# Performance work log

Hardware: AMD Instinct MI355X
Metric: run time of the kernel (lower is better)

## Reference

```python
import jax, jax.numpy as jnp
import numpy as np

N_NODES = 50000
N_EDGES = 800000
D = 128


def setup_inputs() -> dict:
    key = jax.random.key(0)
    ks = jax.random.split(key, 8)
    h = jax.random.normal(ks[0], (N_NODES, D), dtype=jnp.float32)
    src = jax.random.randint(ks[1], (N_EDGES,), 0, N_NODES, dtype=jnp.int64)
    dst = jax.random.randint(ks[2], (N_EDGES,), 0, N_NODES, dtype=jnp.int64)
    # Glorot-ish init for the three GraphConv weights
    scale = 1.0 / np.sqrt(D)
    W0 = jax.random.normal(ks[3], (D, D), dtype=jnp.float32) * scale
    W1 = jax.random.normal(ks[4], (D, D), dtype=jnp.float32) * scale
    W2 = jax.random.normal(ks[5], (D, D), dtype=jnp.float32) * scale
    b0 = jnp.zeros((D,), dtype=jnp.float32)
    b1 = jnp.zeros((D,), dtype=jnp.float32)
    b2 = jnp.zeros((D,), dtype=jnp.float32)
    return {"h": h, "src": src, "dst": dst, "W0": W0, "b0": b0,
            "W1": W1, "b1": b1, "W2": W2, "b2": b2}


def _graph_conv(x, src, dst, W, b, n_nodes):
    """DGL GraphConv, norm='both', activation=ReLU.
    in_feats == out_feats -> aggregate first, then matmul W."""
    ones = jnp.ones_like(src, dtype=x.dtype)
    out_deg = jnp.clip(jax.ops.segment_sum(ones, src, num_segments=n_nodes), 1.0)
    in_deg = jnp.clip(jax.ops.segment_sum(ones, dst, num_segments=n_nodes), 1.0)
    x = x * (out_deg ** -0.5)[:, None]          # src-side normalization
    m = jax.ops.segment_sum(x[src], dst, num_segments=n_nodes)  # sparse aggregation
    m = m * (in_deg ** -0.5)[:, None]           # dst-side normalization
    return jax.nn.relu(m @ W + b)


def reference(h, src, dst, W0, b0, W1, b1, W2, b2):
    n = h.shape[0]
    h = _graph_conv(h, src, dst, W0, b0, n)
    h = _graph_conv(h, src, dst, W1, b1, n)
    h = _graph_conv(h, src, dst, W2, b2, n)
    return h
```

## Files before the change

kernel.cpp:

```cpp
#include <hip/hip_runtime.h>

#define N_NODES 50000
#define N_EDGES 800000
#define D 128
#define CAP 48
#define NPADN 50176

#define PACKB 24

#define ABLK 400
#define AEDGES (N_EDGES / ABLK)
#define DBW 256
#define DNB 196
#define DCAP 6144
#define FNB (2 * DNB)
#define HN 128
#define SBW 512
#define SNB 98
#define BCAP 10240

typedef __attribute__((ext_vector_type(4))) float f32x4;
typedef __attribute__((ext_vector_type(8))) short s16x8;

__device__ inline unsigned short f32_to_bf16_rtne(float f) {
    union { float f; unsigned u; } c; c.f = f;
    unsigned u = c.u;
    u += 0x7FFF + ((u >> 16) & 1);
    return (unsigned short)(u >> 16);
}
__device__ inline float bf16_to_f32(unsigned short h) {
    union { unsigned u; float f; } c; c.u = ((unsigned)h) << 16;
    return c.f;
}
__device__ inline unsigned pack_bf2(float a, float b) {
    return (unsigned)f32_to_bf16_rtne(a) | ((unsigned)f32_to_bf16_rtne(b) << 16);
}
__device__ inline void unpack_bf2(unsigned u, float& a, float& b) {
    union { unsigned u; float f; } c0, c1;
    c0.u = u << 16; c1.u = u & 0xFFFF0000u;
    a = c0.f; b = c1.f;
}
__device__ inline void acc_uint4(uint4 v, float* a) {
    float f0, f1;
    unpack_bf2(v.x, f0, f1); a[0] += f0; a[1] += f1;
    unpack_bf2(v.y, f0, f1); a[2] += f0; a[3] += f1;
    unpack_bf2(v.z, f0, f1); a[4] += f0; a[5] += f1;
    unpack_bf2(v.w, f0, f1); a[6] += f0; a[7] += f1;
}


__global__ __launch_bounds__(256) void build_bin(const int* __restrict__ src,
                                                 const int* __restrict__ dst,
                                                 int* __restrict__ gcurD,
                                                 int* __restrict__ gcurS,
                                                 unsigned long long* __restrict__ dbin,
                                                 unsigned short* __restrict__ sbin,
                                                 const float* __restrict__ W0,
                                                 const float* __restrict__ W1,
                                                 const float* __restrict__ W2,
                                                 s16x8* __restrict__ wpk) {
    int b = blockIdx.x;
    if (b < ABLK) {
        __shared__ int cntD[DNB], baseD[DNB], c2D[DNB];
        __shared__ int cntS[SNB], baseS[SNB], c2S[SNB];
        for (int i = threadIdx.x; i < DNB; i += 256) { cntD[i] = 0; c2D[i] = 0; }
        for (int i = threadIdx.x; i < SNB; i += 256) { cntS[i] = 0; c2S[i] = 0; }
        __syncthreads();
        int e0 = b * AEDGES;
        for (int i = threadIdx.x; i < AEDGES; i += 256) {
            int s = src[e0 + i], d = dst[e0 + i];
            atomicAdd(&cntD[d >> 8], 1);
            atomicAdd(&cntS[s >> 9], 1);
        }
        __syncthreads();
        for (int i = threadIdx.x; i < DNB; i += 256) baseD[i] = atomicAdd(&gcurD[i], cntD[i]);
        for (int i = threadIdx.x; i < SNB; i += 256) baseS[i] = atomicAdd(&gcurS[i], cntS[i]);
        __syncthreads();
        for (int i = threadIdx.x; i < AEDGES; i += 256) {
            int e = e0 + i;
            int s = src[e], d = dst[e];
            int bd = d >> 8;
            int rd = atomicAdd(&c2D[bd], 1);
            int od = baseD[bd] + rd;
            if (od < DCAP)
                dbin[(size_t)bd * DCAP + od] =
                    ((unsigned long long)(unsigned)e << 32) | ((unsigned)(d & 255) << 16) | (unsigned)s;
            int bs = s >> 9;
            int rs = atomicAdd(&c2S[bs], 1);
            int os = baseS[bs] + rs;
            if (os < BCAP) sbin[bs * BCAP + os] = (unsigned short)s;
        }
    } else {
        int wid = (b - ABLK) * 4 + (threadIdx.x >> 6);
        if (wid >= 96) return;
        int lane = threadIdx.x & 63;
        int layer = wid / 32, rem = wid % 32;
        int ct = rem >> 2, ks = rem & 3;
        const float* W = (layer == 0) ? W0 : (layer == 1) ? W1 : W2;
        int col = ct * 16 + (lane & 15);
        int k0  = ks * 32 + (lane >> 4) * 8;
        s16x8 hi, lo;
#pragma unroll
        for (int j = 0; j < 8; j++) {
            float w = W[(k0 + j) * D + col];
            unsigned short h = f32_to_bf16_rtne(w);
            hi[j] = (short)h;
            lo[j] = (short)f32_to_bf16_rtne(w - bf16_to_f32(h));
        }
        int idx = layer * 4096 + (ct * 4 + ks) * 64 + lane;
        wpk[idx]        = hi;
        wpk[idx + 2048] = lo;
    }
}


__global__ __launch_bounds__(256) void fill_sort(const unsigned long long* __restrict__ dbin,
                                                 const int* __restrict__ gcurD,
                                                 unsigned short* __restrict__ slots,
                                                 int* __restrict__ cursor,
                                                 const unsigned short* __restrict__ sbin,
                                                 const int* __restrict__ gcurS,
                                                 int* __restrict__ odeg) {
    __shared__ unsigned key[HN * 49];
    __shared__ unsigned short sv[HN * 48];
    __shared__ unsigned short sv2[HN * 50];
    __shared__ int cur[HN];
    __shared__ int scnt[SBW];
    int b = blockIdx.x;
    if (b < FNB) {
        int bucket = b >> 1, half = b & 1;
        int t = threadIdx.x;
        if (t < HN) cur[t] = 0;
        __syncthreads();
        int n = min(gcurD[bucket], DCAP);
        const unsigned long long* eb = dbin + (size_t)bucket * DCAP;
        for (int i = t; i < n; i += 256) {
            unsigned long long w = eb[i];
            int dl = (int)((w >> 16) & 255);
            if ((dl >> 7) == half) {
                int d2 = dl & (HN - 1);
                int p = atomicAdd(&cur[d2], 1);
                if (p < CAP) {
                    key[d2 * 49 + p] = (unsigned)(w >> 32);
                    sv[d2 * 48 + p] = (unsigned short)(w & 0xFFFFu);
                }
            }
        }
        __syncthreads();
        {
            int node = t & (HN - 1), sub = t >> 7;
            int m = min(cur[node], CAP);
            int kb = node * 49, vb = node * 48, ob = node * 50;
            for (int i = sub; i < m; i += 2) {
                unsigned ki = key[kb + i];
                int r = 0;
#pragma unroll 4
                for (int j = 0; j < m; j++) r += (key[kb + j] < ki) ? 1 : 0;
                sv2[ob + r] = sv[vb + i];
            }
        }
        __syncthreads();
        int n0 = bucket * DBW + half * HN;
        unsigned* dw = (unsigned*)(slots + (size_t)n0 * CAP);
        for (int idx = t; idx < HN * (CAP / 2); idx += 256) {
            int node = idx / (CAP / 2);
            int w2 = idx - node * (CAP / 2);
            dw[idx] = *(const unsigned*)&sv2[node * 50 + w2 * 2];
        }
        if (t < HN) cursor[n0 + t] = cur[t];
    } else {
        int bb = b - FNB;
        for (int i = threadIdx.x; i < SBW; i += 256) scnt[i] = 0;
        __syncthreads();
        int nE = min(gcurS[bb], BCAP);
        const unsigned short* es = sbin + (size_t)bb * BCAP;
        for (int i = threadIdx.x; i < nE; i += 256)
            atomicAdd(&scnt[es[i] & (SBW - 1)], 1);
        __syncthreads();
        int n0 = bb * SBW;
        for (int i = threadIdx.x; i < SBW; i += 256)
            if (n0 + i < N_NODES) odeg[n0 + i] = scnt[i];
    }
}


__global__ __launch_bounds__(256) void hconv(const float4* __restrict__ h,
                                             const int* __restrict__ odeg,
                                             float* __restrict__ s_out,
                                             uint2* __restrict__ hbA,
                                             uint2* __restrict__ hbB) {
    int gid = blockIdx.x * 256 + threadIdx.x;
    const int total = N_NODES * 32;
    if (gid < total) {
        int node = gid >> 5;
        float so = rsqrtf(fmaxf((float)odeg[node], 1.0f));
        if ((gid & 31) == 0) s_out[node] = so;
        float4 v = h[gid];
        hbA[gid] = make_uint2(pack_bf2(so * v.x, so * v.y), pack_bf2(so * v.z, so * v.w));
    } else if (gid < total + 32) {
        hbA[total + (gid - total)] = make_uint2(0u, 0u);
    } else if (gid < total + 64) {
        hbB[total + (gid - total - 32)] = make_uint2(0u, 0u);
    }
}


__global__ __launch_bounds__(256) void fused_layer(const uint4* __restrict__ x,
                                                   const unsigned short* __restrict__ slots,
                                                   const int* __restrict__ deg,
                                                   const s16x8* __restrict__ wpk,
                                                   const float* __restrict__ bias,
                                                   const float* __restrict__ s_out,
                                                   float* __restrict__ outf,
                                                   unsigned short* __restrict__ outb) {
    __shared__ s16x8 mHI[16 * 17];
    __shared__ s16x8 mLO[16 * 17];
    int tid = threadIdx.x;
    int row0 = blockIdx.x * 16;

    {
        int nloc = tid >> 4;
        int l    = tid & 15;
        int node = row0 + nloc;
        int dgraw = deg[node];
        int dg = min(dgraw, CAP);
        int base = node * CAP;
        int idx0 = (l      < dg) ? (int)slots[base + l]      : N_NODES;
        int idx1 = (16 + l < dg) ? (int)slots[base + 16 + l] : N_NODES;
        int idx2 = (32 + l < dg) ? (int)slots[base + 32 + l] : N_NODES;

        float a[8];
#pragma unroll
        for (int j = 0; j < 8; j++) a[j] = 0.f;

        int nr = (dg + 7) >> 3;
        for (int r = 0; r < nr; r++) {
            int c = r >> 1;
            int v = (c == 0) ? idx0 : ((c == 1) ? idx1 : idx2);
            int k = (r & 1) * 8;
            int s0 = __shfl(v, k + 0, 16), s1 = __shfl(v, k + 1, 16);
            int s2 = __shfl(v, k + 2, 16), s3 = __shfl(v, k + 3, 16);
            int s4 = __shfl(v, k + 4, 16), s5 = __shfl(v, k + 5, 16);
            int s6 = __shfl(v, k + 6, 16), s7 = __shfl(v, k + 7, 16);
            uint4 g0 = x[s0 * 16 + l];
            uint4 g1 = x[s1 * 16 + l];
            uint4 g2 = x[s2 * 16 + l];
            uint4 g3 = x[s3 * 16 + l];
            uint4 g4 = x[s4 * 16 + l];
            uint4 g5 = x[s5 * 16 + l];
            uint4 g6 = x[s6 * 16 + l];
            uint4 g7 = x[s7 * 16 + l];
            acc_uint4(g0, a); acc_uint4(g1, a); acc_uint4(g2, a); acc_uint4(g3, a);
            acc_uint4(g4, a); acc_uint4(g5, a); acc_uint4(g6, a); acc_uint4(g7, a);
        }
        float si = rsqrtf(fmaxf((float)dgraw, 1.0f));
        s16x8 ahi, alo;
#pragma unroll
        for (int j = 0; j < 8; j++) {
            float av = a[j] * si;
            unsigned short hh = f32_to_bf16_rtne(av);
            ahi[j] = (short)hh;
            alo[j] = (short)f32_to_bf16_rtne(av - bf16_to_f32(hh));
        }
        mHI[nloc * 17 + l] = ahi;
        mLO[nloc * 17 + l] = alo;
    }
    __syncthreads();

    int wv = tid >> 6;
    int lane = tid & 63;
    int arow = lane & 15, aq = lane >> 4;
    int ct0 = wv * 2, ct1 = ct0 + 1;
    f32x4 acc0 = (f32x4)0.f, acc1 = (f32x4)0.f;

#pragma unroll
    for (int ks = 0; ks < 4; ks++) {
        s16x8 ahi = mHI[arow * 17 + ks * 4 + aq];
        s16x8 alo = mLO[arow * 17 + ks * 4 + aq];
        int idx0 = (ct0 * 4 + ks) * 64 + lane;
        int idx1 = (ct1 * 4 + ks) * 64 + lane;
        s16x8 b0h = wpk[idx0], b0l = wpk[idx0 + 2048];
        s16x8 b1h = wpk[idx1], b1l = wpk[idx1 + 2048];
        acc0 = __builtin_amdgcn_mfma_f32_16x16x32_bf16(ahi, b0h, acc0, 0, 0, 0);
        acc0 = __builtin_amdgcn_mfma_f32_16x16x32_bf16(alo, b0h, acc0, 0, 0, 0);
        acc0 = __builtin_amdgcn_mfma_f32_16x16x32_bf16(ahi, b0l, acc0, 0, 0, 0);
        acc1 = __builtin_amdgcn_mfma_f32_16x16x32_bf16(ahi, b1h, acc1, 0, 0, 0);
        acc1 = __builtin_amdgcn_mfma_f32_16x16x32_bf16(alo, b1h, acc1, 0, 0, 0);
        acc1 = __builtin_amdgcn_mfma_f32_16x16x32_bf16(ahi, b1l, acc1, 0, 0, 0);
    }

    int crow0 = aq * 4;
    float so4[4];
    if (outb) {
#pragma unroll
        for (int r = 0; r < 4; r++) so4[r] = s_out[row0 + crow0 + r];
    }
    int colA = ct0 * 16 + arow, colB = ct1 * 16 + arow;
    float bA = bias[colA], bB = bias[colB];
#pragma unroll
    for (int r = 0; r < 4; r++) {
        size_t rowoff = (size_t)(row0 + crow0 + r) * D;
        float vA = fmaxf(acc0[r] + bA, 0.f);
        float vB = fmaxf(acc1[r] + bB, 0.f);
        if (outf) { outf[rowoff + colA] = vA; outf[rowoff + colB] = vB; }
        if (outb) {
            outb[rowoff + colA] = f32_to_bf16_rtne(so4[r] * vA);
            outb[rowoff + colB] = f32_to_bf16_rtne(so4[r] * vB);
        }
    }
}


extern "C" void kernel_launch(void* const* d_in, const int* in_sizes, int n_in,
                              void* d_out, int out_size, void* d_ws, size_t ws_size,
                              hipStream_t stream) {
    const float* h  = (const float*)d_in[0];
    const int*  src = (const int*)d_in[1];
    const int*  dst = (const int*)d_in[2];
    const float* W0 = (const float*)d_in[3];
    const float* b0 = (const float*)d_in[4];
    const float* W1 = (const float*)d_in[5];
    const float* b1 = (const float*)d_in[6];
    const float* W2 = (const float*)d_in[7];
    const float* b2 = (const float*)d_in[8];
    float* out = (float*)d_out;

    char* w = (char*)d_ws;
    auto carve = [&](size_t bytes) -> void* {
        void* p = (void*)w;
        w += (bytes + 255) & ~(size_t)255;
        return p;
    };
    int*      gcurD   = (int*)carve((DNB + 128) * sizeof(int));
    int*      gcurS   = gcurD + DNB;
    int*      cursor  = (int*)carve(NPADN * sizeof(int));
    int*      odeg    = (int*)carve(N_NODES * sizeof(int));
    float*    s_out   = (float*)carve(N_NODES * sizeof(float));
    unsigned long long* dbin = (unsigned long long*)carve((size_t)DNB * DCAP * 8);
    unsigned short* slots = (unsigned short*)carve((size_t)NPADN * CAP * sizeof(unsigned short));
    unsigned short* sbin  = (unsigned short*)carve((size_t)SNB * BCAP * sizeof(unsigned short));
    unsigned short* actA  = (unsigned short*)carve((size_t)(N_NODES + 1) * D * 2);
    unsigned short* actB  = (unsigned short*)carve((size_t)(N_NODES + 1) * D * 2);
    s16x8*    wpk     = (s16x8*)carve(3 * 4096 * sizeof(s16x8));

    hipMemsetAsync(gcurD, 0, (DNB + 128) * sizeof(int), stream);
    build_bin<<<ABLK + PACKB, 256, 0, stream>>>(src, dst, gcurD, gcurS, dbin, sbin,
                                                W0, W1, W2, wpk);
    fill_sort<<<FNB + SNB, 256, 0, stream>>>(dbin, gcurD, slots, cursor,
                                             sbin, gcurS, odeg);
    hconv<<<(N_NODES * 32 + 64 + 255) / 256, 256, 0, stream>>>((const float4*)h, odeg, s_out,
                                                               (uint2*)actA, (uint2*)actB);

    const int GRID = N_NODES / 16;

    fused_layer<<<GRID, 256, 0, stream>>>((const uint4*)actA, slots, cursor,
                                          wpk, b0, s_out, nullptr, actB);
    fused_layer<<<GRID, 256, 0, stream>>>((const uint4*)actB, slots, cursor,
                                          wpk + 4096, b1, s_out, nullptr, actA);
    fused_layer<<<GRID, 256, 0, stream>>>((const uint4*)actA, slots, cursor,
                                          wpk + 8192, b2, s_out, out, nullptr);
}
```

Before: 234.0 us.

## Fuse hconv into fill_sort and sort neighbor slots by source id

```diff
diff --git a/kernel.cpp b/kernel.cpp
--- a/kernel.cpp
+++ b/kernel.cpp
@@ -15,6 +15,8 @@
 #define DCAP 6144
 #define FNB (2 * DNB)
 #define HN 128
+#define SSTR 51
+#define OSTR 52
 #define SBW 512
 #define SNB 98
 #define BCAP 10240
@@ -53,7 +55,7 @@
                                                  const int* __restrict__ dst,
                                                  int* __restrict__ gcurD,
                                                  int* __restrict__ gcurS,
-                                                 unsigned long long* __restrict__ dbin,
+                                                 unsigned* __restrict__ dbin,
                                                  unsigned short* __restrict__ sbin,
                                                  const float* __restrict__ W0,
                                                  const float* __restrict__ W1,
@@ -83,8 +85,7 @@
             int rd = atomicAdd(&c2D[bd], 1);
             int od = baseD[bd] + rd;
             if (od < DCAP)
-                dbin[(size_t)bd * DCAP + od] =
-                    ((unsigned long long)(unsigned)e << 32) | ((unsigned)(d & 255) << 16) | (unsigned)s;
+                dbin[(size_t)bd * DCAP + od] = ((unsigned)(d & 255) << 16) | (unsigned)s;
             int bs = s >> 9;
             int rs = atomicAdd(&c2S[bs], 1);
             int os = baseS[bs] + rs;
@@ -114,49 +115,51 @@
 }
 
 
-__global__ __launch_bounds__(256) void fill_sort(const unsigned long long* __restrict__ dbin,
+__global__ __launch_bounds__(256) void fill_sort(const unsigned* __restrict__ dbin,
                                                  const int* __restrict__ gcurD,
                                                  unsigned short* __restrict__ slots,
                                                  int* __restrict__ cursor,
                                                  const unsigned short* __restrict__ sbin,
                                                  const int* __restrict__ gcurS,
-                                                 int* __restrict__ odeg) {
-    __shared__ unsigned key[HN * 49];
-    __shared__ unsigned short sv[HN * 48];
-    __shared__ unsigned short sv2[HN * 50];
+                                                 const float4* __restrict__ h,
+                                                 float* __restrict__ s_out,
+                                                 uint2* __restrict__ hbA,
+                                                 uint2* __restrict__ hbB) {
+    __shared__ unsigned short sv[HN * SSTR];
+    __shared__ unsigned short sv2[HN * OSTR];
     __shared__ int cur[HN];
     __shared__ int scnt[SBW];
     int b = blockIdx.x;
+    int t = threadIdx.x;
     if (b < FNB) {
         int bucket = b >> 1, half = b & 1;
-        int t = threadIdx.x;
         if (t < HN) cur[t] = 0;
         __syncthreads();
         int n = min(gcurD[bucket], DCAP);
-        const unsigned long long* eb = dbin + (size_t)bucket * DCAP;
+        const unsigned* eb = dbin + (size_t)bucket * DCAP;
         for (int i = t; i < n; i += 256) {
-            unsigned long long w = eb[i];
-            int dl = (int)((w >> 16) & 255);
+            unsigned w = eb[i];
+            int dl = (int)(w >> 16);
             if ((dl >> 7) == half) {
                 int d2 = dl & (HN - 1);
                 int p = atomicAdd(&cur[d2], 1);
-                if (p < CAP) {
-                    key[d2 * 49 + p] = (unsigned)(w >> 32);
-                    sv[d2 * 48 + p] = (unsigned short)(w & 0xFFFFu);
-                }
+                if (p < CAP) sv[d2 * SSTR + p] = (unsigned short)(w & 0xFFFFu);
             }
         }
         __syncthreads();
         {
             int node = t & (HN - 1), sub = t >> 7;
             int m = min(cur[node], CAP);
-            int kb = node * 49, vb = node * 48, ob = node * 50;
+            int vb = node * SSTR, ob = node * OSTR;
             for (int i = sub; i < m; i += 2) {
-                unsigned ki = key[kb + i];
+                unsigned vi = sv[vb + i];
                 int r = 0;
 #pragma unroll 4
-                for (int j = 0; j < m; j++) r += (key[kb + j] < ki) ? 1 : 0;
-                sv2[ob + r] = sv[vb + i];
+                for (int j = 0; j < m; j++) {
+                    unsigned vj = sv[vb + j];
+                    r += (vj < vi || (vj == vi && j < i)) ? 1 : 0;
+                }
+                sv2[ob + r] = (unsigned short)vi;
             }
         }
         __syncthreads();
@@ -165,42 +168,33 @@
         for (int idx = t; idx < HN * (CAP / 2); idx += 256) {
             int node = idx / (CAP / 2);
             int w2 = idx - node * (CAP / 2);
-            dw[idx] = *(const unsigned*)&sv2[node * 50 + w2 * 2];
+            dw[idx] = *(const unsigned*)&sv2[node * OSTR + w2 * 2];
         }
         if (t < HN) cursor[n0 + t] = cur[t];
-    } else {
+    } else if (b < FNB + SNB) {
         int bb = b - FNB;
-        for (int i = threadIdx.x; i < SBW; i += 256) scnt[i] = 0;
+        for (int i = t; i < SBW; i += 256) scnt[i] = 0;
         __syncthreads();
         int nE = min(gcurS[bb], BCAP);
         const unsigned short* es = sbin + (size_t)bb * BCAP;
-        for (int i = threadIdx.x; i < nE; i += 256)
+        for (int i = t; i < nE; i += 256)
             atomicAdd(&scnt[es[i] & (SBW - 1)], 1);
         __syncthreads();
         int n0 = bb * SBW;
-        for (int i = threadIdx.x; i < SBW; i += 256)
-            if (n0 + i < N_NODES) odeg[n0 + i] = scnt[i];
-    }
-}
-
-
-__global__ __launch_bounds__(256) void hconv(const float4* __restrict__ h,
-                                             const int* __restrict__ odeg,
-                                             float* __restrict__ s_out,
-                                             uint2* __restrict__ hbA,
-                                             uint2* __restrict__ hbB) {
-    int gid = blockIdx.x * 256 + threadIdx.x;
-    const int total = N_NODES * 32;
-    if (gid < total) {
-        int node = gid >> 5;
-        float so = rsqrtf(fmaxf((float)odeg[node], 1.0f));
-        if ((gid & 31) == 0) s_out[node] = so;
-        float4 v = h[gid];
-        hbA[gid] = make_uint2(pack_bf2(so * v.x, so * v.y), pack_bf2(so * v.z, so * v.w));
-    } else if (gid < total + 32) {
-        hbA[total + (gid - total)] = make_uint2(0u, 0u);
-    } else if (gid < total + 64) {
-        hbB[total + (gid - total - 32)] = make_uint2(0u, 0u);
+        for (int i = t; i < SBW * 32; i += 256) {
+            int nl = i >> 5;
+            int node = n0 + nl;
+            if (node < N_NODES) {
+                float so = rsqrtf(fmaxf((float)scnt[nl], 1.0f));
+                if ((i & 31) == 0) s_out[node] = so;
+                int gid = node * 32 + (i & 31);
+                float4 v = h[gid];
+                hbA[gid] = make_uint2(pack_bf2(so * v.x, so * v.y), pack_bf2(so * v.z, so * v.w));
+            }
+        }
+    } else {
+        if (t < 32) hbA[N_NODES * 32 + t] = make_uint2(0u, 0u);
+        else if (t < 64) hbB[N_NODES * 32 + (t - 32)] = make_uint2(0u, 0u);
     }
 }
 
@@ -334,9 +328,8 @@
     int*      gcurD   = (int*)carve((DNB + 128) * sizeof(int));
     int*      gcurS   = gcurD + DNB;
     int*      cursor  = (int*)carve(NPADN * sizeof(int));
-    int*      odeg    = (int*)carve(N_NODES * sizeof(int));
     float*    s_out   = (float*)carve(N_NODES * sizeof(float));
-    unsigned long long* dbin = (unsigned long long*)carve((size_t)DNB * DCAP * 8);
+    unsigned* dbin    = (unsigned*)carve((size_t)DNB * DCAP * 4);
     unsigned short* slots = (unsigned short*)carve((size_t)NPADN * CAP * sizeof(unsigned short));
     unsigned short* sbin  = (unsigned short*)carve((size_t)SNB * BCAP * sizeof(unsigned short));
     unsigned short* actA  = (unsigned short*)carve((size_t)(N_NODES + 1) * D * 2);
@@ -346,10 +339,9 @@
     hipMemsetAsync(gcurD, 0, (DNB + 128) * sizeof(int), stream);
     build_bin<<<ABLK + PACKB, 256, 0, stream>>>(src, dst, gcurD, gcurS, dbin, sbin,
                                                 W0, W1, W2, wpk);
-    fill_sort<<<FNB + SNB, 256, 0, stream>>>(dbin, gcurD, slots, cursor,
-                                             sbin, gcurS, odeg);
-    hconv<<<(N_NODES * 32 + 64 + 255) / 256, 256, 0, stream>>>((const float4*)h, odeg, s_out,
-                                                               (uint2*)actA, (uint2*)actB);
+    fill_sort<<<FNB + SNB + 1, 256, 0, stream>>>(dbin, gcurD, slots, cursor,
+                                                 sbin, gcurS, (const float4*)h,
+                                                 s_out, (uint2*)actA, (uint2*)actB);
 
     const int GRID = N_NODES / 16;
 
```

Result: slower. 249.9 us (+6.8%).
